# Kernel tuning notes

Measured on AMD Instinct MI355X. Metric: run time of the kernel, lower is better.

Reference implementation:

```python
import jax, jax.numpy as jnp
import numpy as np

B, N, C = 2, 2048, 1024
H = 16
R = 4
MLP = 4096
LORA_SCALE = 1.0 / R  # lora_alpha=1, r=4
EPS = 1e-5


def _ln(x, g, b):
    m = jnp.mean(x, axis=-1, keepdims=True)
    v = jnp.mean(jnp.square(x - m), axis=-1, keepdims=True)
    return (x - m) * jax.lax.rsqrt(v + EPS) * g + b


def setup_inputs() -> dict:
    key = jax.random.key(0)
    ks = jax.random.split(key, 16)
    s = lambda k, shape, fan: jax.random.normal(k, shape, jnp.float32) * (1.0 / np.sqrt(fan))
    return {
        "x": jax.random.normal(ks[0], (B, N, C), jnp.float32),
        "pos": jax.random.normal(ks[1], (B, N, C), jnp.float32),
        "Wqkv": s(ks[2], (3 * C, C), C),
        "b_qkv": jnp.zeros((3 * C,), jnp.float32),
        "lora_A": s(ks[3], (2 * R, C), C),          # rows 0:R -> q, R:2R -> v
        "lora_B": s(ks[4], (2 * C, R), R) * 0.1,     # rows 0:C -> q, C:2C -> v
        "Wproj": s(ks[5], (C, C), C),
        "b_proj": jnp.zeros((C,), jnp.float32),
        "ln1_g": jnp.ones((C,), jnp.float32),
        "ln1_b": jnp.zeros((C,), jnp.float32),
        "ln2_g": jnp.ones((C,), jnp.float32),
        "ln2_b": jnp.zeros((C,), jnp.float32),
        "W1": s(ks[6], (MLP, C), C),
        "b1": jnp.zeros((MLP,), jnp.float32),
        "W2": s(ks[7], (C, MLP), MLP),
        "b2": jnp.zeros((C,), jnp.float32),
        "idx": 0,
    }


def reference(x, pos, Wqkv, b_qkv, lora_A, lora_B, Wproj, b_proj,
              ln1_g, ln1_b, ln2_g, ln2_b, W1, b1, W2, b2, idx):
    # (dropout layers are identity in eval mode)
    x = x + pos

    # --- attention block: Residual(PreNormDrop(SelfAttention)) ---
    h = _ln(x, ln1_g, ln1_b)                              # [B,N,C]
    qkv = h @ Wqkv.T + b_qkv                              # [B,N,3C]
    # LoRA MergedLinear: low-rank update on q and v thirds only
    after_A = h @ lora_A.T                                # [B,N,2R]
    dq = after_A[..., :R] @ lora_B[:C].T * LORA_SCALE     # [B,N,C]
    dv = after_A[..., R:] @ lora_B[C:].T * LORA_SCALE     # [B,N,C]
    qkv = qkv.at[..., :C].add(dq).at[..., 2 * C:].add(dv)

    Dh = C // H
    q, k, v = [t.reshape(B, N, H, Dh).transpose(0, 2, 1, 3)
               for t in jnp.split(qkv, 3, axis=-1)]       # each [B,H,N,Dh]
    scale = Dh ** -0.5
    attn = jnp.einsum('bhid,bhjd->bhij', q, k) * scale    # [B,H,N,N]
    attn = jax.nn.softmax(attn, axis=-1)
    o = jnp.einsum('bhij,bhjd->bhid', attn, v)            # [B,H,N,Dh]
    o = o.transpose(0, 2, 1, 3).reshape(B, N, C)
    o = o @ Wproj.T + b_proj
    x = x + o

    # --- FFN block: Residual(PreNorm(FeedForward)) ---
    h2 = _ln(x, ln2_g, ln2_b)
    h2 = jax.nn.gelu(h2 @ W1.T + b1, approximate=False)
    h2 = h2 @ W2.T + b2
    return x + h2
```

## Files before the change

### kernel.cpp

```cpp
#include <hip/hip_runtime.h>
#include <hip/hip_bf16.h>
#include <math.h>

typedef __hip_bfloat16 bf16;
typedef __attribute__((ext_vector_type(4))) float f32x4;
typedef __attribute__((ext_vector_type(16))) float f32x16;
typedef __attribute__((ext_vector_type(8))) short s16x8;

__device__ __forceinline__ void async_cp16(void* lds, const void* g) {
    __builtin_amdgcn_global_load_lds((const __attribute__((address_space(1))) void*)g,
                                     (__attribute__((address_space(3))) void*)lds, 16, 0, 0);
}

__global__ __launch_bounds__(256)
void cvt_all(const float* __restrict__ w0, const float* __restrict__ w1,
             const float* __restrict__ w2, const float* __restrict__ w3,
             bf16* __restrict__ o0, bf16* __restrict__ o1,
             bf16* __restrict__ o2, bf16* __restrict__ o3) {
    int i = blockIdx.x * 256 + threadIdx.x;
    const float* src; bf16* dst; int j = i;
    if (j < 786432)            { src = w0; dst = o0; }
    else if (j < 1048576)      { j -= 786432;  src = w1; dst = o1; }
    else if (j < 2097152)      { j -= 1048576; src = w2; dst = o2; }
    else                       { j -= 2097152; src = w3; dst = o3; }
    float4 v = ((const float4*)src)[j];
    union { bf16 o[4]; uint2 u; } pk;
    pk.o[0] = __float2bfloat16(v.x); pk.o[1] = __float2bfloat16(v.y);
    pk.o[2] = __float2bfloat16(v.z); pk.o[3] = __float2bfloat16(v.w);
    ((uint2*)dst)[j] = pk.u;
}

template <bool ADD>
__global__ __launch_bounds__(256)
void ln_kernel(const float* __restrict__ xin, const float* __restrict__ pos,
               const float* __restrict__ gam, const float* __restrict__ bet,
               float* __restrict__ x1, bf16* __restrict__ hout) {
    const int row = blockIdx.x, tid = threadIdx.x;
    const size_t off = (size_t)row * 1024;
    float4 v = ((const float4*)(xin + off))[tid];
    if constexpr (ADD) {
        float4 p = ((const float4*)(pos + off))[tid];
        v.x += p.x; v.y += p.y; v.z += p.z; v.w += p.w;
        ((float4*)(x1 + off))[tid] = v;
    }
    float s  = v.x + v.y + v.z + v.w;
    float s2 = v.x*v.x + v.y*v.y + v.z*v.z + v.w*v.w;
#pragma unroll
    for (int o = 32; o >= 1; o >>= 1) { s += __shfl_xor(s, o); s2 += __shfl_xor(s2, o); }
    __shared__ float sS[4], sS2[4];
    int w = tid >> 6, lane = tid & 63;
    if (lane == 0) { sS[w] = s; sS2[w] = s2; }
    __syncthreads();
    float mean = (sS[0] + sS[1] + sS[2] + sS[3]) * (1.f / 1024.f);
    float e2   = (sS2[0] + sS2[1] + sS2[2] + sS2[3]) * (1.f / 1024.f);
    float rstd = rsqrtf(e2 - mean * mean + 1e-5f);
    float4 gv = ((const float4*)gam)[tid], bv = ((const float4*)bet)[tid];
    bf16* ho = hout + off + tid * 4;
    ho[0] = __float2bfloat16((v.x - mean) * rstd * gv.x + bv.x);
    ho[1] = __float2bfloat16((v.y - mean) * rstd * gv.y + bv.y);
    ho[2] = __float2bfloat16((v.z - mean) * rstd * gv.z + bv.z);
    ho[3] = __float2bfloat16((v.w - mean) * rstd * gv.w + bv.w);
}

template <int MODE>
__global__ __launch_bounds__(256)
void gemm_bt(const bf16* __restrict__ A, const bf16* __restrict__ B,
             const float* __restrict__ bias, void* __restrict__ outp,
             int M, int N, int K) {
    __shared__ bf16 As[128 * 32];
    __shared__ bf16 Bs[128 * 32];
    const int tid = threadIdx.x;
    const int lane = tid & 63, w = tid >> 6;
    const int grp = lane >> 4, c16 = lane & 15;
    const int wm = (w & 1) * 64, wn = (w >> 1) * 64;
    const int bm = blockIdx.y * 128, bn = blockIdx.x * 128;

    f32x4 acc[4][4];
    const f32x4 zero = {0.f, 0.f, 0.f, 0.f};
#pragma unroll
    for (int mi = 0; mi < 4; mi++)
#pragma unroll
        for (int ni = 0; ni < 4; ni++) acc[mi][ni] = zero;

    for (int k0 = 0; k0 < K; k0 += 32) {
#pragma unroll
        for (int t = 0; t < 2; t++) {
            int s = t * 256 + tid;
            int row = s >> 2, blks = s & 3;
            int gblk = blks ^ ((row >> 1) & 3);
            async_cp16(&As[s * 8], A + (size_t)(bm + row) * K + k0 + gblk * 8);
            async_cp16(&Bs[s * 8], B + (size_t)(bn + row) * K + k0 + gblk * 8);
        }
        __syncthreads();
        s16x8 af[4], bf[4];
#pragma unroll
        for (int mi = 0; mi < 4; mi++) {
            int r = wm + mi * 16 + c16;
            af[mi] = *(const s16x8*)&As[r * 32 + ((grp ^ ((r >> 1) & 3)) << 3)];
        }
#pragma unroll
        for (int ni = 0; ni < 4; ni++) {
            int r = wn + ni * 16 + c16;
            bf[ni] = *(const s16x8*)&Bs[r * 32 + ((grp ^ ((r >> 1) & 3)) << 3)];
        }
#pragma unroll
        for (int mi = 0; mi < 4; mi++)
#pragma unroll
            for (int ni = 0; ni < 4; ni++)
                acc[mi][ni] = __builtin_amdgcn_mfma_f32_16x16x32_bf16(af[mi], bf[ni], acc[mi][ni], 0, 0, 0);
        __syncthreads();
    }

#pragma unroll
    for (int mi = 0; mi < 4; mi++)
#pragma unroll
        for (int ni = 0; ni < 4; ni++) {
            int r0 = bm + wm + mi * 16 + grp * 4;
            int c  = bn + wn + ni * 16 + c16;
            float bv = bias[c];
#pragma unroll
            for (int q = 0; q < 4; q++) {
                size_t idx = (size_t)(r0 + q) * N + c;
                float v = acc[mi][ni][q] + bv;
                if constexpr (MODE == 0) {
                    ((float*)outp)[idx] = v;
                } else {
                    v = 0.5f * v * (1.0f + erff(v * 0.70710678118f));
                    ((bf16*)outp)[idx] = __float2bfloat16(v);
                }
            }
        }
}

__global__ __launch_bounds__(256)
void gemm_n64(const bf16* __restrict__ A, const bf16* __restrict__ B,
              const float* __restrict__ bias, const float* __restrict__ resid,
              float* __restrict__ outp, int M, int N, int K) {
    __shared__ bf16 As[128 * 64];
    __shared__ bf16 Bs[64 * 64];
    const int tid = threadIdx.x;
    const int lane = tid & 63, w = tid >> 6;
    const int grp = lane >> 4, c16 = lane & 15;
    const int wm = w * 32;
    const int bm = blockIdx.y * 128, bn = blockIdx.x * 64;

    f32x4 acc[2][4];
    const f32x4 zero = {0.f, 0.f, 0.f, 0.f};
#pragma unroll
    for (int mi = 0; mi < 2; mi++)
#pragma unroll
        for (int ni = 0; ni < 4; ni++) acc[mi][ni] = zero;

    for (int k0 = 0; k0 < K; k0 += 64) {
#pragma unroll
        for (int t = 0; t < 4; t++) {
            int s = t * 256 + tid;
            int row = s >> 3, db = s & 7;
            async_cp16(&As[s * 8], A + (size_t)(bm + row) * K + k0 + ((db ^ (row & 7)) << 3));
        }
#pragma unroll
        for (int t = 0; t < 2; t++) {
            int s = t * 256 + tid;
            int row = s >> 3, db = s & 7;
            async_cp16(&Bs[s * 8], B + (size_t)(bn + row) * K + k0 + ((db ^ (row & 7)) << 3));
        }
        __syncthreads();
#pragma unroll
        for (int kc = 0; kc < 2; kc++) {
            s16x8 af[2], bf[4];
#pragma unroll
            for (int mi = 0; mi < 2; mi++) {
                int r = wm + mi * 16 + c16;
                af[mi] = *(const s16x8*)&As[r * 64 + ((((kc << 2) | grp) ^ (r & 7)) << 3)];
            }
#pragma unroll
            for (int ni = 0; ni < 4; ni++) {
                int rb = ni * 16 + c16;
                bf[ni] = *(const s16x8*)&Bs[rb * 64 + ((((kc << 2) | grp) ^ (rb & 7)) << 3)];
            }
#pragma unroll
            for (int mi = 0; mi < 2; mi++)
#pragma unroll
                for (int ni = 0; ni < 4; ni++)
                    acc[mi][ni] = __builtin_amdgcn_mfma_f32_16x16x32_bf16(af[mi], bf[ni], acc[mi][ni], 0, 0, 0);
        }
        __syncthreads();
    }

#pragma unroll
    for (int mi = 0; mi < 2; mi++)
#pragma unroll
        for (int ni = 0; ni < 4; ni++) {
            int r0 = bm + wm + mi * 16 + grp * 4;
            int c  = bn + ni * 16 + c16;
            float bv = bias[c];
#pragma unroll
            for (int q = 0; q < 4; q++) {
                size_t idx = (size_t)(r0 + q) * N + c;
                outp[idx] = acc[mi][ni][q] + bv + resid[idx];
            }
        }
}

__global__ __launch_bounds__(256)
void lora_a_kernel(const bf16* __restrict__ h, const float* __restrict__ A,
                   float* __restrict__ afterA) {
    const int row = blockIdx.x, tid = threadIdx.x;
    float hv[4];
#pragma unroll
    for (int t = 0; t < 4; t++) hv[t] = __bfloat162float(h[(size_t)row * 1024 + tid * 4 + t]);
    float p[8];
#pragma unroll
    for (int r = 0; r < 8; r++) {
        float4 av = ((const float4*)(A + (size_t)r * 1024))[tid];
        p[r] = hv[0] * av.x + hv[1] * av.y + hv[2] * av.z + hv[3] * av.w;
    }
#pragma unroll
    for (int r = 0; r < 8; r++)
#pragma unroll
        for (int o = 32; o >= 1; o >>= 1) p[r] += __shfl_xor(p[r], o);
    __shared__ float red[4][8];
    int w = tid >> 6, lane = tid & 63;
    if (lane == 0) {
#pragma unroll
        for (int r = 0; r < 8; r++) red[w][r] = p[r];
    }
    __syncthreads();
    if (tid < 8) afterA[(size_t)row * 8 + tid] = red[0][tid] + red[1][tid] + red[2][tid] + red[3][tid];
}

__global__ __launch_bounds__(256)
void attn_prep(const float* __restrict__ qkv, const float* __restrict__ afterA,
               const float* __restrict__ loraB, bf16* __restrict__ Qb,
               bf16* __restrict__ Kb, bf16* __restrict__ Vt) {
    const int bh = blockIdx.y, b = bh >> 4, h = bh & 15;
    const int it = blockIdx.x;
    __shared__ bf16 Vs[64 * 65];
    const int tid = threadIdx.x;
#pragma unroll
    for (int t = 0; t < 16; t++) {
        int s = t * 256 + tid;
        int il = s >> 6, d = s & 63;
        int ig = b * 2048 + it * 64 + il;
        size_t grow = (size_t)ig * 3072 + h * 64 + d;
        int col = h * 64 + d;
        const float* aA = afterA + (size_t)ig * 8;
        float4 bq = ((const float4*)loraB)[col];
        float4 bvv = ((const float4*)loraB)[1024 + col];
        float dq = (aA[0]*bq.x  + aA[1]*bq.y  + aA[2]*bq.z  + aA[3]*bq.w)  * 0.25f;
        float dv = (aA[4]*bvv.x + aA[5]*bvv.y + aA[6]*bvv.z + aA[7]*bvv.w) * 0.25f;
        float q = (qkv[grow] + dq) * 0.125f;
        float k = qkv[grow + 1024];
        float v = qkv[grow + 2048] + dv;
        size_t orow = (size_t)(bh * 2048 + it * 64 + il) * 64 + d;
        Qb[orow] = __float2bfloat16(q);
        Kb[orow] = __float2bfloat16(k);
        Vs[d * 65 + il] = __float2bfloat16(v);
    }
    __syncthreads();
#pragma unroll
    for (int t = 0; t < 16; t++) {
        int s = t * 256 + tid;
        int d = s >> 6, il = s & 63;
        Vt[(size_t)(bh * 64 + d) * 2048 + it * 64 + il] = Vs[d * 65 + il];
    }
}

__global__ __launch_bounds__(256)
void attn_fused(const bf16* __restrict__ Qb, const bf16* __restrict__ Kb,
                const bf16* __restrict__ Vt, bf16* __restrict__ Og) {
    __shared__ bf16 Qs[128 * 64], Ks[64 * 64], Vs[64 * 64];
    const int tid = threadIdx.x;
    const int lane = tid & 63, w = tid >> 6;
    const int c32 = lane & 31, l5 = lane >> 5;
    const int bh = blockIdx.y, b = bh >> 4, h = bh & 15;
    const int i0 = blockIdx.x * 128;
    const int rowperm = (c32 & 19) | (((c32 >> 3) & 1) << 2) | (((c32 >> 2) & 1) << 3);

    const size_t qbase = (size_t)(bh * 2048 + i0) * 64;
#pragma unroll
    for (int t = 0; t < 4; t++) {
        int s = t * 256 + tid;
        int row = s >> 3, db = s & 7;
        async_cp16(&Qs[s * 8], Qb + qbase + row * 64 + ((db ^ (row & 7)) << 3));
    }
    __syncthreads();
    s16x8 qf[4];
    {
        int rq = w * 32 + c32;
#pragma unroll
        for (int kc = 0; kc < 4; kc++) {
            int db = 2 * kc + l5;
            qf[kc] = *(const s16x8*)&Qs[rq * 64 + ((db ^ (rq & 7)) << 3)];
        }
    }

    f32x16 Oq[2];
#pragma unroll
    for (int dq = 0; dq < 2; dq++)
#pragma unroll
        for (int r = 0; r < 16; r++) Oq[dq][r] = 0.f;
    float m_i = -3.0e38f, l_i = 0.f;

    for (int j0 = 0; j0 < 2048; j0 += 64) {
        __syncthreads();
#pragma unroll
        for (int t = 0; t < 2; t++) {
            int s = t * 256 + tid;
            int row = s >> 3, db = s & 7;
            int gb = db ^ (row & 7);
            async_cp16(&Ks[s * 8], Kb + (size_t)(bh * 2048 + j0 + row) * 64 + gb * 8);
            async_cp16(&Vs[s * 8], Vt + (size_t)(bh * 64 + row) * 2048 + j0 + gb * 8);
        }
        __syncthreads();

        f32x16 Sq[2];
#pragma unroll
        for (int jq = 0; jq < 2; jq++) {
#pragma unroll
            for (int r = 0; r < 16; r++) Sq[jq][r] = 0.f;
            int rk = jq * 32 + rowperm;
#pragma unroll
            for (int kc = 0; kc < 4; kc++) {
                int db = 2 * kc + l5;
                s16x8 af = *(const s16x8*)&Ks[rk * 64 + ((db ^ (rk & 7)) << 3)];
                Sq[jq] = __builtin_amdgcn_mfma_f32_32x32x16_bf16(af, qf[kc], Sq[jq], 0, 0, 0);
            }
        }

        float mx = Sq[0][0];
#pragma unroll
        for (int r = 1; r < 16; r++) mx = fmaxf(mx, Sq[0][r]);
#pragma unroll
        for (int r = 0; r < 16; r++) mx = fmaxf(mx, Sq[1][r]);
        mx = fmaxf(mx, __shfl_xor(mx, 32));
        float mn = fmaxf(m_i, mx);
        float alpha = __expf(m_i - mn);
        float rs = 0.f;
#pragma unroll
        for (int jq = 0; jq < 2; jq++)
#pragma unroll
            for (int r = 0; r < 16; r++) {
                float p = __expf(Sq[jq][r] - mn);
                Sq[jq][r] = p; rs += p;
            }
        rs += __shfl_xor(rs, 32);
        m_i = mn;
        l_i = l_i * alpha + rs;

        s16x8 pf[4];
#pragma unroll
        for (int kc = 0; kc < 4; kc++) {
            union { s16x8 v; bf16 e[8]; } u;
#pragma unroll
            for (int jj = 0; jj < 8; jj++)
                u.e[jj] = __float2bfloat16(Sq[kc >> 1][8 * (kc & 1) + jj]);
            pf[kc] = u.v;
        }

#pragma unroll
        for (int dq = 0; dq < 2; dq++)
#pragma unroll
            for (int r = 0; r < 16; r++) Oq[dq][r] *= alpha;

#pragma unroll
        for (int dq = 0; dq < 2; dq++) {
            int rd = dq * 32 + c32;
#pragma unroll
            for (int kc = 0; kc < 4; kc++) {
                int jb = 2 * kc + l5;
                s16x8 af = *(const s16x8*)&Vs[rd * 64 + ((jb ^ (rd & 7)) << 3)];
                Oq[dq] = __builtin_amdgcn_mfma_f32_32x32x16_bf16(af, pf[kc], Oq[dq], 0, 0, 0);
            }
        }
    }

    float inv = 1.0f / l_i;
    int i = i0 + w * 32 + c32;
    size_t obase = (size_t)(b * 2048 + i) * 1024 + h * 64;
#pragma unroll
    for (int dq = 0; dq < 2; dq++)
#pragma unroll
        for (int rg = 0; rg < 4; rg++) {
            union { bf16 e[4]; uint2 u; } pk;
#pragma unroll
            for (int c = 0; c < 4; c++)
                pk.e[c] = __float2bfloat16(Oq[dq][rg * 4 + c] * inv);
            int d0 = dq * 32 + l5 * 4 + rg * 8;
            *(uint2*)&Og[obase + d0] = pk.u;
        }
}

extern "C" void kernel_launch(void* const* d_in, const int* in_sizes, int n_in,
                              void* d_out, int out_size, void* d_ws, size_t ws_size,
                              hipStream_t stream) {
    const float* x     = (const float*)d_in[0];
    const float* pos   = (const float*)d_in[1];
    const float* Wqkv  = (const float*)d_in[2];
    const float* bqkv  = (const float*)d_in[3];
    const float* loraA = (const float*)d_in[4];
    const float* loraB = (const float*)d_in[5];
    const float* Wproj = (const float*)d_in[6];
    const float* bproj = (const float*)d_in[7];
    const float* ln1g  = (const float*)d_in[8];
    const float* ln1b  = (const float*)d_in[9];
    const float* ln2g  = (const float*)d_in[10];
    const float* ln2b  = (const float*)d_in[11];
    const float* W1    = (const float*)d_in[12];
    const float* b1    = (const float*)d_in[13];
    const float* W2    = (const float*)d_in[14];
    const float* b2    = (const float*)d_in[15];

    char* ws = (char*)d_ws;
    float* x1     = (float*)(ws + 0);
    bf16*  hbuf   = (bf16*) (ws + 16777216);
    float* qkv    = (float*)(ws + 25165824);
    bf16*  gbuf   = (bf16*) (ws + 25165824);
    float* afterA = (float*)(ws + 75497472);
    bf16*  Qb     = (bf16*) (ws + 75628544);
    bf16*  Kb     = (bf16*) (ws + 84017152);
    bf16*  Vt     = (bf16*) (ws + 92405760);
    bf16*  Obf    = (bf16*) (ws + 100794368);
    bf16*  Wqkvb  = (bf16*) (ws + 109182976);
    bf16*  Wprojb = (bf16*) (ws + 115474432);
    bf16*  W1b    = (bf16*) (ws + 117571584);
    bf16*  W2b    = (bf16*) (ws + 125960192);

    cvt_all<<<12288, 256, 0, stream>>>(Wqkv, Wproj, W1, W2, Wqkvb, Wprojb, W1b, W2b);

    ln_kernel<true><<<4096, 256, 0, stream>>>(x, pos, ln1g, ln1b, x1, hbuf);

    gemm_bt<0><<<dim3(24, 32), 256, 0, stream>>>(hbuf, Wqkvb, bqkv, qkv, 4096, 3072, 1024);

    lora_a_kernel<<<4096, 256, 0, stream>>>(hbuf, loraA, afterA);

    attn_prep<<<dim3(32, 32), 256, 0, stream>>>(qkv, afterA, loraB, Qb, Kb, Vt);
    attn_fused<<<dim3(16, 32), 256, 0, stream>>>(Qb, Kb, Vt, Obf);

    gemm_n64<<<dim3(16, 32), 256, 0, stream>>>(Obf, Wprojb, bproj, x1, x1, 4096, 1024, 1024);

    ln_kernel<false><<<4096, 256, 0, stream>>>(x1, nullptr, ln2g, ln2b, nullptr, hbuf);

    gemm_bt<2><<<dim3(32, 32), 256, 0, stream>>>(hbuf, W1b, b1, gbuf, 4096, 4096, 1024);

    gemm_n64<<<dim3(16, 32), 256, 0, stream>>>(gbuf, W2b, b2, x1, (float*)d_out, 4096, 1024, 4096);

    (void)in_sizes; (void)n_in; (void)out_size; (void)ws_size;
}
```

Measured before the change: 432.7 us.

## Use BK=64 GEMM tiles, bf16 QKV output, and tanh-approx GELU

The QKV and FFN1 GEMMs now load 64-wide K tiles into LDS with an 8-way XOR swizzle. This halves the number of barrier pairs per K sweep and does two MFMA sub-steps per load. The QKV projection now writes bf16 instead of fp32, which halves its store traffic and the read traffic in attn_prep, at the cost of rounding QKV before the LoRA add. The exact erf GELU is replaced by a tanh approximation built on __expf, which is cheaper but deviates slightly from the reference.

```diff
diff --git a/kernel.cpp b/kernel.cpp
--- a/kernel.cpp
+++ b/kernel.cpp
@@ -10,6 +10,13 @@
 __device__ __forceinline__ void async_cp16(void* lds, const void* g) {
     __builtin_amdgcn_global_load_lds((const __attribute__((address_space(1))) void*)g,
                                      (__attribute__((address_space(3))) void*)lds, 16, 0, 0);
+}
+
+__device__ __forceinline__ float gelu_fast(float x) {
+    float y = 1.5957691216f * (x + 0.044715f * x * x * x);
+    float t = __expf(y);
+    float th = 1.0f - 2.0f / (t + 1.0f);
+    return 0.5f * x * (1.0f + th);
 }
 
 __global__ __launch_bounds__(256)
@@ -64,11 +71,11 @@
 
 template <int MODE>
 __global__ __launch_bounds__(256)
-void gemm_bt(const bf16* __restrict__ A, const bf16* __restrict__ B,
-             const float* __restrict__ bias, void* __restrict__ outp,
-             int M, int N, int K) {
-    __shared__ bf16 As[128 * 32];
-    __shared__ bf16 Bs[128 * 32];
+void gemm_bk64(const bf16* __restrict__ A, const bf16* __restrict__ B,
+               const float* __restrict__ bias, bf16* __restrict__ outp,
+               int M, int N, int K) {
+    __shared__ bf16 As[128 * 64];
+    __shared__ bf16 Bs[128 * 64];
     const int tid = threadIdx.x;
     const int lane = tid & 63, w = tid >> 6;
     const int grp = lane >> 4, c16 = lane & 15;
@@ -82,32 +89,35 @@
 #pragma unroll
         for (int ni = 0; ni < 4; ni++) acc[mi][ni] = zero;
 
-    for (int k0 = 0; k0 < K; k0 += 32) {
-#pragma unroll
-        for (int t = 0; t < 2; t++) {
+    for (int k0 = 0; k0 < K; k0 += 64) {
+#pragma unroll
+        for (int t = 0; t < 4; t++) {
             int s = t * 256 + tid;
-            int row = s >> 2, blks = s & 3;
-            int gblk = blks ^ ((row >> 1) & 3);
-            async_cp16(&As[s * 8], A + (size_t)(bm + row) * K + k0 + gblk * 8);
-            async_cp16(&Bs[s * 8], B + (size_t)(bn + row) * K + k0 + gblk * 8);
-        }
-        __syncthreads();
-        s16x8 af[4], bf[4];
-#pragma unroll
-        for (int mi = 0; mi < 4; mi++) {
-            int r = wm + mi * 16 + c16;
-            af[mi] = *(const s16x8*)&As[r * 32 + ((grp ^ ((r >> 1) & 3)) << 3)];
-        }
-#pragma unroll
-        for (int ni = 0; ni < 4; ni++) {
-            int r = wn + ni * 16 + c16;
-            bf[ni] = *(const s16x8*)&Bs[r * 32 + ((grp ^ ((r >> 1) & 3)) << 3)];
-        }
-#pragma unroll
-        for (int mi = 0; mi < 4; mi++)
-#pragma unroll
-            for (int ni = 0; ni < 4; ni++)
-                acc[mi][ni] = __builtin_amdgcn_mfma_f32_16x16x32_bf16(af[mi], bf[ni], acc[mi][ni], 0, 0, 0);
+            int row = s >> 3, db = s & 7;
+            int gb = (db ^ (row & 7)) << 3;
+            async_cp16(&As[s * 8], A + (size_t)(bm + row) * K + k0 + gb);
+            async_cp16(&Bs[s * 8], B + (size_t)(bn + row) * K + k0 + gb);
+        }
+        __syncthreads();
+#pragma unroll
+        for (int kc = 0; kc < 2; kc++) {
+            s16x8 af[4], bf[4];
+#pragma unroll
+            for (int mi = 0; mi < 4; mi++) {
+                int r = wm + mi * 16 + c16;
+                af[mi] = *(const s16x8*)&As[r * 64 + ((((kc << 2) | grp) ^ (r & 7)) << 3)];
+            }
+#pragma unroll
+            for (int ni = 0; ni < 4; ni++) {
+                int r = wn + ni * 16 + c16;
+                bf[ni] = *(const s16x8*)&Bs[r * 64 + ((((kc << 2) | grp) ^ (r & 7)) << 3)];
+            }
+#pragma unroll
+            for (int mi = 0; mi < 4; mi++)
+#pragma unroll
+                for (int ni = 0; ni < 4; ni++)
+                    acc[mi][ni] = __builtin_amdgcn_mfma_f32_16x16x32_bf16(af[mi], bf[ni], acc[mi][ni], 0, 0, 0);
+        }
         __syncthreads();
     }
 
@@ -122,12 +132,8 @@
             for (int q = 0; q < 4; q++) {
                 size_t idx = (size_t)(r0 + q) * N + c;
                 float v = acc[mi][ni][q] + bv;
-                if constexpr (MODE == 0) {
-                    ((float*)outp)[idx] = v;
-                } else {
-                    v = 0.5f * v * (1.0f + erff(v * 0.70710678118f));
-                    ((bf16*)outp)[idx] = __float2bfloat16(v);
-                }
+                if constexpr (MODE == 2) v = gelu_fast(v);
+                outp[idx] = __float2bfloat16(v);
             }
         }
 }
@@ -230,7 +236,7 @@
 }
 
 __global__ __launch_bounds__(256)
-void attn_prep(const float* __restrict__ qkv, const float* __restrict__ afterA,
+void attn_prep(const bf16* __restrict__ qkv, const float* __restrict__ afterA,
                const float* __restrict__ loraB, bf16* __restrict__ Qb,
                bf16* __restrict__ Kb, bf16* __restrict__ Vt) {
     const int bh = blockIdx.y, b = bh >> 4, h = bh & 15;
@@ -249,9 +255,9 @@
         float4 bvv = ((const float4*)loraB)[1024 + col];
         float dq = (aA[0]*bq.x  + aA[1]*bq.y  + aA[2]*bq.z  + aA[3]*bq.w)  * 0.25f;
         float dv = (aA[4]*bvv.x + aA[5]*bvv.y + aA[6]*bvv.z + aA[7]*bvv.w) * 0.25f;
-        float q = (qkv[grow] + dq) * 0.125f;
-        float k = qkv[grow + 1024];
-        float v = qkv[grow + 2048] + dv;
+        float q = (__bfloat162float(qkv[grow]) + dq) * 0.125f;
+        float k = __bfloat162float(qkv[grow + 1024]);
+        float v = __bfloat162float(qkv[grow + 2048]) + dv;
         size_t orow = (size_t)(bh * 2048 + it * 64 + il) * 64 + d;
         Qb[orow] = __float2bfloat16(q);
         Kb[orow] = __float2bfloat16(k);
@@ -414,23 +420,23 @@
     char* ws = (char*)d_ws;
     float* x1     = (float*)(ws + 0);
     bf16*  hbuf   = (bf16*) (ws + 16777216);
-    float* qkv    = (float*)(ws + 25165824);
-    bf16*  gbuf   = (bf16*) (ws + 25165824);
-    float* afterA = (float*)(ws + 75497472);
-    bf16*  Qb     = (bf16*) (ws + 75628544);
-    bf16*  Kb     = (bf16*) (ws + 84017152);
-    bf16*  Vt     = (bf16*) (ws + 92405760);
-    bf16*  Obf    = (bf16*) (ws + 100794368);
-    bf16*  Wqkvb  = (bf16*) (ws + 109182976);
-    bf16*  Wprojb = (bf16*) (ws + 115474432);
-    bf16*  W1b    = (bf16*) (ws + 117571584);
-    bf16*  W2b    = (bf16*) (ws + 125960192);
+    bf16*  qkv    = (bf16*) (ws + 25165824);
+    bf16*  gbuf   = (bf16*) (ws + 50331648);
+    float* afterA = (float*)(ws + 83886080);
+    bf16*  Qb     = (bf16*) (ws + 84017152);
+    bf16*  Kb     = (bf16*) (ws + 92405760);
+    bf16*  Vt     = (bf16*) (ws + 100794368);
+    bf16*  Obf    = (bf16*) (ws + 109182976);
+    bf16*  Wqkvb  = (bf16*) (ws + 117571584);
+    bf16*  Wprojb = (bf16*) (ws + 123863040);
+    bf16*  W1b    = (bf16*) (ws + 125960192);
+    bf16*  W2b    = (bf16*) (ws + 134348800);
 
     cvt_all<<<12288, 256, 0, stream>>>(Wqkv, Wproj, W1, W2, Wqkvb, Wprojb, W1b, W2b);
 
     ln_kernel<true><<<4096, 256, 0, stream>>>(x, pos, ln1g, ln1b, x1, hbuf);
 
-    gemm_bt<0><<<dim3(24, 32), 256, 0, stream>>>(hbuf, Wqkvb, bqkv, qkv, 4096, 3072, 1024);
+    gemm_bk64<0><<<dim3(24, 32), 256, 0, stream>>>(hbuf, Wqkvb, bqkv, qkv, 4096, 3072, 1024);
 
     lora_a_kernel<<<4096, 256, 0, stream>>>(hbuf, loraA, afterA);
 
@@ -441,7 +447,7 @@
 
     ln_kernel<false><<<4096, 256, 0, stream>>>(x1, nullptr, ln2g, ln2b, nullptr, hbuf);
 
-    gemm_bt<2><<<dim3(32, 32), 256, 0, stream>>>(hbuf, W1b, b1, gbuf, 4096, 4096, 1024);
+    gemm_bk64<2><<<dim3(32, 32), 256, 0, stream>>>(hbuf, W1b, b1, gbuf, 4096, 4096, 1024);
 
     gemm_n64<<<dim3(16, 32), 256, 0, stream>>>(gbuf, W2b, b2, x1, (float*)d_out, 4096, 1024, 4096);
 
```

Result: faster. 409.6 us (-5.3%).
